# Kernel optimization log

Hardware: AMD Instinct MI355X
Metric: run time of the kernel (lower is better)

The kernel has to match this reference:

```python
import jax, jax.numpy as jnp
from jax import lax
import numpy as np

EPS = 1e-5

def _conv_bn(x, w, g, b, m, v):
    # 3x3 VALID conv (no bias) + inference BatchNorm, no relu
    y = lax.conv_general_dilated(x, w, window_strides=(1, 1), padding='VALID',
                                 dimension_numbers=('NCHW', 'OIHW', 'NCHW'))
    inv = g * lax.rsqrt(v + EPS)                      # [C]
    return y * inv[None, :, None, None] + (b - m * inv)[None, :, None, None]

def _xcorr_depthwise(z, x):
    # z: [B,C,hz,wz] kernel, x: [B,C,hx,wx] search -> [B,C,hx-hz+1,wx-wz+1]
    C = z.shape[1]
    def one(zi, xi):
        return lax.conv_general_dilated(xi[None], zi[:, None], (1, 1), 'VALID',
                                        dimension_numbers=('NCHW', 'OIHW', 'NCHW'),
                                        feature_group_count=C)[0]
    return jax.vmap(one)(z, x)

def setup_inputs() -> dict:
    key = jax.random.key(0)
    B, Cin, H = 32, 256, 256
    ks = jax.random.split(key, 30)
    d = {
        'z': jax.random.normal(ks[0], (B, Cin, 8, 8), jnp.float32),
        'x': jax.random.normal(ks[1], (B, Cin, 32, 32), jnp.float32),
    }
    i = 2
    for p in ['cls_z', 'cls_x', 'reg_z', 'reg_x']:
        d[p + '_w'] = 0.01 * jax.random.normal(ks[i], (H, Cin, 3, 3), jnp.float32); i += 1
        d[p + '_g'] = jnp.ones((H,), jnp.float32)
        d[p + '_b'] = jnp.zeros((H,), jnp.float32)
        d[p + '_m'] = 0.1 * jax.random.normal(ks[i], (H,), jnp.float32); i += 1
        d[p + '_v'] = jax.random.uniform(ks[i], (H,), jnp.float32, 0.5, 1.5); i += 1
    return d

def reference(z, x,
              cls_z_w, cls_z_g, cls_z_b, cls_z_m, cls_z_v,
              cls_x_w, cls_x_g, cls_x_b, cls_x_m, cls_x_v,
              reg_z_w, reg_z_g, reg_z_b, reg_z_m, reg_z_v,
              reg_x_w, reg_x_g, reg_x_b, reg_x_m, reg_x_v):
    cls_z = _conv_bn(z, cls_z_w, cls_z_g, cls_z_b, cls_z_m, cls_z_v)
    cls_x = _conv_bn(x, cls_x_w, cls_x_g, cls_x_b, cls_x_m, cls_x_v)
    cls_out = _xcorr_depthwise(cls_z, cls_x)
    reg_z = _conv_bn(z, reg_z_w, reg_z_g, reg_z_b, reg_z_m, reg_z_v)
    reg_x = _conv_bn(x, reg_x_w, reg_x_g, reg_x_b, reg_x_m, reg_x_v)
    reg_out = _xcorr_depthwise(reg_z, reg_x)
    return (cls_out, reg_out)
```

## Files before the change

### kernel.cpp

```cpp
#include <hip/hip_runtime.h>

#define EPS 1e-5f

typedef __attribute__((ext_vector_type(8))) short bf16x8;
typedef __attribute__((ext_vector_type(4))) float f32x4;
typedef __attribute__((ext_vector_type(4))) unsigned short u16x4;
typedef unsigned short ushort_t;

__device__ __forceinline__ ushort_t f2bf(float f) {
  unsigned u = __float_as_uint(f);
  unsigned r = (u + 0x7fffu + ((u >> 16) & 1u)) >> 16;
  return (ushort_t)r;
}
__device__ __forceinline__ float bf2f(ushort_t h) {
  return __uint_as_float((unsigned)h << 16);
}

#define GLDS16(g, l) __builtin_amdgcn_global_load_lds( \
    (const __attribute__((address_space(1))) void*)(g), \
    (__attribute__((address_space(3))) void*)(l), 16, 0, 0)

__global__ __launch_bounds__(256) void pack_kernel(
    const float* __restrict__ x, const float* __restrict__ z,
    const float* __restrict__ wxa, const float* __restrict__ wxb,
    const float* __restrict__ wza, const float* __restrict__ wzb,
    ushort_t* __restrict__ xh, ushort_t* __restrict__ zh,
    ushort_t* __restrict__ Bxo, ushort_t* __restrict__ Bzo)
{
  __shared__ ushort_t t[256 * 66];
  int id = blockIdx.x;
  int tid = threadIdx.x;
  if (id < 1024) {
    int b = id >> 5, h = id & 31;
    const float* src = x + (size_t)b * 256 * 1024 + h * 32;
#pragma unroll
    for (int it = 0; it < 32; ++it) {
      int f = it * 256 + tid;
      int c = f >> 5, w = f & 31;
      t[c * 34 + w] = f2bf(src[c * 1024 + w]);
    }
    __syncthreads();
    ushort_t* dst = xh + (size_t)(b * 32 + h) * 32 * 256;
#pragma unroll
    for (int it = 0; it < 32; ++it) {
      int f = it * 256 + tid;
      int w = f >> 8, c = f & 255;
      dst[w * 256 + c] = t[c * 34 + w];
    }
  } else if (id < 1056) {
    int b = id - 1024;
    const float* src = z + (size_t)b * 256 * 64;
#pragma unroll
    for (int it = 0; it < 64; ++it) {
      int f = it * 256 + tid;
      int c = f >> 6, hw = f & 63;
      t[c * 66 + hw] = f2bf(src[c * 64 + hw]);
    }
    __syncthreads();
    ushort_t* dst = zh + (size_t)b * 64 * 256;
#pragma unroll
    for (int it = 0; it < 64; ++it) {
      int f = it * 256 + tid;
      int hw = f >> 8, c = f & 255;
      dst[hw * 256 + c] = t[c * 66 + hw];
    }
  } else {
    int wid = id - 1056;
    int isZ = wid >> 9;
    int n   = wid & 511;
    const float* s0 = isZ ? wza : wxa;
    const float* s1 = isZ ? wzb : wxb;
    const float* src = (n < 256 ? s0 : s1) + (size_t)(n & 255) * 2304 + tid * 9;
    ushort_t* dst = (isZ ? Bzo : Bxo) + (size_t)n * 2304 + tid;
#pragma unroll
    for (int tap = 0; tap < 9; ++tap)
      dst[tap * 256] = f2bf(src[tap]);
  }
}

template<int OW, int OWH, int IW, int IMG, typename OutT>
__device__ __forceinline__ void conv_body(
    int mtile, int ntile,
    const ushort_t* __restrict__ Aimg, const ushort_t* __restrict__ Bw,
    const float* __restrict__ g0, const float* __restrict__ b0,
    const float* __restrict__ m0, const float* __restrict__ v0,
    const float* __restrict__ g1, const float* __restrict__ b1,
    const float* __restrict__ m1, const float* __restrict__ v1,
    OutT* __restrict__ out0, OutT* __restrict__ out1,
    ushort_t* As, ushort_t* Bs)
{
  const int tid  = threadIdx.x;
  const int lane = tid & 63;
  const int wave = tid >> 6;
  const int wr   = wave >> 1, wc = wave & 1;

  const int chunk = (tid & 7) ^ ((tid >> 3) & 7);
  int abase[4], bbase[4];
#pragma unroll
  for (int i = 0; i < 4; ++i) {
    int row = i * 32 + (tid >> 3);
    int m_g = mtile * 128 + row;
    int b   = m_g / OWH;
    int s   = m_g - b * OWH;
    int oh  = s / OW;
    int ow  = s - oh * OW;
    abase[i] = (b * IMG + oh * IW + ow) * 256 + chunk * 8;
    int n_g = ntile * 128 + row;
    bbase[i] = n_g * 2304 + chunk * 8;
  }

  f32x4 acc[4][4];
#pragma unroll
  for (int i = 0; i < 4; ++i)
#pragma unroll
    for (int j = 0; j < 4; ++j)
      acc[i][j] = (f32x4){0.f, 0.f, 0.f, 0.f};

  const int lrow = lane & 15;
  const int lk   = lane >> 4;
  const int rA   = wr * 64;
  const int rB   = wc * 64;
  const int sw   = lrow & 7;

  for (int ks = 0; ks < 36; ++ks) {
    const int k0  = ks * 64;
    const int tap = k0 >> 8;
    const int ci0 = k0 & 255;
    const int kh  = tap / 3;
    const int kw  = tap - kh * 3;
    const int aoff = (kh * IW + kw) * 256 + ci0;
#pragma unroll
    for (int i = 0; i < 4; ++i) {
      GLDS16(Aimg + abase[i] + aoff, &As[(i * 256 + tid) * 8]);
      GLDS16(Bw + bbase[i] + k0,     &Bs[(i * 256 + tid) * 8]);
    }
    __syncthreads();
#pragma unroll
    for (int kc = 0; kc < 2; ++kc) {
      bf16x8 af[4], bfr[4];
#pragma unroll
      for (int mi = 0; mi < 4; ++mi)
        af[mi] = *(const bf16x8*)&As[(rA + mi * 16 + lrow) * 64 + (((kc << 2) | lk) ^ sw) * 8];
#pragma unroll
      for (int ni = 0; ni < 4; ++ni)
        bfr[ni] = *(const bf16x8*)&Bs[(rB + ni * 16 + lrow) * 64 + (((kc << 2) | lk) ^ sw) * 8];
#pragma unroll
      for (int mi = 0; mi < 4; ++mi)
#pragma unroll
        for (int ni = 0; ni < 4; ++ni)
          acc[mi][ni] = __builtin_amdgcn_mfma_f32_16x16x32_bf16(
              af[mi], bfr[ni], acc[mi][ni], 0, 0, 0);
    }
    __syncthreads();
  }

#pragma unroll
  for (int ni = 0; ni < 4; ++ni) {
    int n_g  = ntile * 128 + rB + ni * 16 + lrow;
    int path = n_g >> 8;
    int co   = n_g & 255;
    const float* G  = path ? g1 : g0;
    const float* Bb = path ? b1 : b0;
    const float* Mm = path ? m1 : m0;
    const float* Vv = path ? v1 : v0;
    float iv = G[co] * rsqrtf(Vv[co] + EPS);
    float be = Bb[co] - Mm[co] * iv;
    OutT* outp = path ? out1 : out0;
#pragma unroll
    for (int mi = 0; mi < 4; ++mi) {
      int m_g = mtile * 128 + rA + mi * 16 + lk * 4;
      int b   = m_g / OWH;
      int s   = m_g - b * OWH;
      if constexpr (sizeof(OutT) == 2) {
        u16x4 pk;
#pragma unroll
        for (int r = 0; r < 4; ++r) pk[r] = f2bf(acc[mi][ni][r] * iv + be);
        *reinterpret_cast<u16x4*>(&outp[(size_t)(b * 256 + co) * OWH + s]) = pk;
      } else {
        f32x4 pk;
#pragma unroll
        for (int r = 0; r < 4; ++r) pk[r] = acc[mi][ni][r] * iv + be;
        *reinterpret_cast<f32x4*>(&outp[(size_t)(b * 256 + co) * OWH + s]) = pk;
      }
    }
  }
}

__global__ __launch_bounds__(256) void conv_fused_kernel(
    const ushort_t* __restrict__ xh, const ushort_t* __restrict__ zh,
    const ushort_t* __restrict__ Bx, const ushort_t* __restrict__ Bz,
    const float* Gcx, const float* Bcx, const float* Mcx, const float* Vcx,
    const float* Grx, const float* Brx, const float* Mrx, const float* Vrx,
    const float* Gcz, const float* Bcz, const float* Mcz, const float* Vcz,
    const float* Grz, const float* Brz, const float* Mrz, const float* Vrz,
    ushort_t* __restrict__ cls_xf, ushort_t* __restrict__ reg_xf,
    float* __restrict__ cls_zf, float* __restrict__ reg_zf)
{
  __shared__ ushort_t As[128 * 64];
  __shared__ ushort_t Bs[128 * 64];
  int id = blockIdx.x;
  if (id < 900) {
    conv_body<30, 900, 32, 1024, ushort_t>(id >> 2, id & 3, xh, Bx,
        Gcx, Bcx, Mcx, Vcx, Grx, Brx, Mrx, Vrx, cls_xf, reg_xf, As, Bs);
  } else {
    int j = id - 900;
    conv_body<6, 36, 8, 64, float>(j >> 2, j & 3, zh, Bz,
        Gcz, Bcz, Mcz, Vcz, Grz, Brz, Mrz, Vrz, cls_zf, reg_zf, As, Bs);
  }
}

__global__ __launch_bounds__(256) void xcorr_kernel(
    const float* __restrict__ cls_zf, const float* __restrict__ reg_zf,
    const ushort_t* __restrict__ cls_xf, const ushort_t* __restrict__ reg_xf,
    float* __restrict__ out)
{
  int id   = blockIdx.x;
  int path = id >> 13;
  int bc   = id & 8191;
  int tid  = threadIdx.x;
  __shared__ float sz[36];
  __shared__ float sx[900];
  const float*    zp = (path ? reg_zf : cls_zf) + (size_t)bc * 36;
  const ushort_t* xp = (path ? reg_xf : cls_xf) + (size_t)bc * 900;
  const unsigned* xp32 = reinterpret_cast<const unsigned*>(xp);
  for (int i = tid; i < 450; i += 256) {
    unsigned u = xp32[i];
    sx[2 * i]     = bf2f((ushort_t)(u & 0xffff));
    sx[2 * i + 1] = bf2f((ushort_t)(u >> 16));
  }
  if (tid < 36) sz[tid] = zp[tid];
  __syncthreads();
  float* op = out + (size_t)path * 5120000 + (size_t)bc * 625;
  for (int pos = tid; pos < 625; pos += 256) {
    int p = pos / 25, q = pos % 25;
    float acc = 0.f;
#pragma unroll
    for (int u = 0; u < 6; ++u)
#pragma unroll
      for (int v = 0; v < 6; ++v)
        acc += sz[u * 6 + v] * sx[(p + u) * 30 + (q + v)];
    op[pos] = acc;
  }
}

extern "C" void kernel_launch(void* const* d_in, const int* in_sizes, int n_in,
                              void* d_out, int out_size, void* d_ws, size_t ws_size,
                              hipStream_t stream) {
  const float* z = (const float*)d_in[0];
  const float* x = (const float*)d_in[1];
  const float *W[4], *G[4], *Bb[4], *M[4], *V[4];
  for (int p = 0; p < 4; ++p) {
    W[p]  = (const float*)d_in[2 + p * 5 + 0];
    G[p]  = (const float*)d_in[2 + p * 5 + 1];
    Bb[p] = (const float*)d_in[2 + p * 5 + 2];
    M[p]  = (const float*)d_in[2 + p * 5 + 3];
    V[p]  = (const float*)d_in[2 + p * 5 + 4];
  }

  char* ws = (char*)d_ws;
  ushort_t* xhwc   = (ushort_t*)ws; ws += (size_t)32*32*32*256 * 2;
  ushort_t* zhwc   = (ushort_t*)ws; ws += (size_t)32*8*8*256 * 2;
  ushort_t* Bx     = (ushort_t*)ws; ws += (size_t)512*2304 * 2;
  ushort_t* Bz     = (ushort_t*)ws; ws += (size_t)512*2304 * 2;
  ushort_t* cls_xf = (ushort_t*)ws; ws += (size_t)32*256*900 * 2;
  ushort_t* reg_xf = (ushort_t*)ws; ws += (size_t)32*256*900 * 2;
  float* cls_zf    = (float*)ws;    ws += (size_t)32*256*36 * 4;
  float* reg_zf    = (float*)ws;

  float* outF = (float*)d_out;

  pack_kernel<<<2080, 256, 0, stream>>>(x, z, W[1], W[3], W[0], W[2],
                                        xhwc, zhwc, Bx, Bz);
  conv_fused_kernel<<<936, 256, 0, stream>>>(
      xhwc, zhwc, Bx, Bz,
      G[1], Bb[1], M[1], V[1], G[3], Bb[3], M[3], V[3],
      G[0], Bb[0], M[0], V[0], G[2], Bb[2], M[2], V[2],
      cls_xf, reg_xf, cls_zf, reg_zf);
  xcorr_kernel<<<16384, 256, 0, stream>>>(cls_zf, reg_zf, cls_xf, reg_xf, outF);
}
```

Measured before the change: 277.6 us.

## Vectorize pack transposes, swizzle conv blocks across XCDs, register-cache xcorr kernel

```diff
diff --git a/kernel.cpp b/kernel.cpp
--- a/kernel.cpp
+++ b/kernel.cpp
@@ -27,54 +27,77 @@
     ushort_t* __restrict__ xh, ushort_t* __restrict__ zh,
     ushort_t* __restrict__ Bxo, ushort_t* __restrict__ Bzo)
 {
-  __shared__ ushort_t t[256 * 66];
+  __shared__ ushort_t t[64 * 260];
   int id = blockIdx.x;
   int tid = threadIdx.x;
   if (id < 1024) {
     int b = id >> 5, h = id & 31;
-    const float* src = x + (size_t)b * 256 * 1024 + h * 32;
-#pragma unroll
-    for (int it = 0; it < 32; ++it) {
+    const float* src = x + (size_t)b * 262144 + h * 32;
+#pragma unroll
+    for (int it = 0; it < 8; ++it) {
       int f = it * 256 + tid;
-      int c = f >> 5, w = f & 31;
-      t[c * 34 + w] = f2bf(src[c * 1024 + w]);
-    }
-    __syncthreads();
-    ushort_t* dst = xh + (size_t)(b * 32 + h) * 32 * 256;
-#pragma unroll
-    for (int it = 0; it < 32; ++it) {
-      int f = it * 256 + tid;
-      int w = f >> 8, c = f & 255;
-      dst[w * 256 + c] = t[c * 34 + w];
+      int c = f >> 3, wq = f & 7;
+      float4 v = *reinterpret_cast<const float4*>(src + c * 1024 + wq * 4);
+      t[(4 * wq + 0) * 260 + c] = f2bf(v.x);
+      t[(4 * wq + 1) * 260 + c] = f2bf(v.y);
+      t[(4 * wq + 2) * 260 + c] = f2bf(v.z);
+      t[(4 * wq + 3) * 260 + c] = f2bf(v.w);
+    }
+    __syncthreads();
+    ushort_t* dst = xh + (size_t)(b * 32 + h) * 8192;
+#pragma unroll
+    for (int it = 0; it < 8; ++it) {
+      int Q = it * 256 + tid;
+      int w = Q >> 6, c0 = (Q & 63) * 4;
+      u16x4 pk = *reinterpret_cast<const u16x4*>(&t[w * 260 + c0]);
+      *reinterpret_cast<u16x4*>(&dst[w * 256 + c0]) = pk;
     }
   } else if (id < 1056) {
     int b = id - 1024;
-    const float* src = z + (size_t)b * 256 * 64;
-#pragma unroll
-    for (int it = 0; it < 64; ++it) {
+    const float* src = z + (size_t)b * 16384;
+#pragma unroll
+    for (int it = 0; it < 16; ++it) {
       int f = it * 256 + tid;
-      int c = f >> 6, hw = f & 63;
-      t[c * 66 + hw] = f2bf(src[c * 64 + hw]);
-    }
-    __syncthreads();
-    ushort_t* dst = zh + (size_t)b * 64 * 256;
-#pragma unroll
-    for (int it = 0; it < 64; ++it) {
-      int f = it * 256 + tid;
-      int hw = f >> 8, c = f & 255;
-      dst[hw * 256 + c] = t[c * 66 + hw];
+      int c = f >> 4, hq = f & 15;
+      float4 v = *reinterpret_cast<const float4*>(src + c * 64 + hq * 4);
+      t[(4 * hq + 0) * 260 + c] = f2bf(v.x);
+      t[(4 * hq + 1) * 260 + c] = f2bf(v.y);
+      t[(4 * hq + 2) * 260 + c] = f2bf(v.z);
+      t[(4 * hq + 3) * 260 + c] = f2bf(v.w);
+    }
+    __syncthreads();
+    ushort_t* dst = zh + (size_t)b * 16384;
+#pragma unroll
+    for (int it = 0; it < 16; ++it) {
+      int Q = it * 256 + tid;
+      int hw = Q >> 6, c0 = (Q & 63) * 4;
+      u16x4 pk = *reinterpret_cast<const u16x4*>(&t[hw * 260 + c0]);
+      *reinterpret_cast<u16x4*>(&dst[hw * 256 + c0]) = pk;
     }
   } else {
+    float* tf = reinterpret_cast<float*>(t);
     int wid = id - 1056;
     int isZ = wid >> 9;
     int n   = wid & 511;
     const float* s0 = isZ ? wza : wxa;
     const float* s1 = isZ ? wzb : wxb;
-    const float* src = (n < 256 ? s0 : s1) + (size_t)(n & 255) * 2304 + tid * 9;
-    ushort_t* dst = (isZ ? Bzo : Bxo) + (size_t)n * 2304 + tid;
-#pragma unroll
-    for (int tap = 0; tap < 9; ++tap)
-      dst[tap * 256] = f2bf(src[tap]);
+    const float* src = (n < 256 ? s0 : s1) + (size_t)(n & 255) * 2304;
+#pragma unroll
+    for (int it = 0; it < 3; ++it) {
+      int f = it * 256 + tid;
+      if (f < 576) {
+        float4 v = *reinterpret_cast<const float4*>(src + f * 4);
+        *reinterpret_cast<float4*>(&tf[f * 4]) = v;
+      }
+    }
+    __syncthreads();
+    ushort_t* dst = (isZ ? Bzo : Bxo) + (size_t)n * 2304;
+#pragma unroll
+    for (int it = 0; it < 9; ++it) {
+      int k = it * 256 + tid;
+      int tap = k >> 8, ci = k & 255;
+      dst[k] = f2bf(tf[ci * 9 + tap]);
+    }
   }
 }
 
@@ -198,12 +221,14 @@
 {
   __shared__ ushort_t As[128 * 64];
   __shared__ ushort_t Bs[128 * 64];
-  int id = blockIdx.x;
-  if (id < 900) {
+  int bid = blockIdx.x;
+  if (bid < 900) {
+    int xcd = bid & 7, within = bid >> 3;
+    int id = (xcd < 4 ? xcd * 113 : 452 + (xcd - 4) * 112) + within;
     conv_body<30, 900, 32, 1024, ushort_t>(id >> 2, id & 3, xh, Bx,
         Gcx, Bcx, Mcx, Vcx, Grx, Brx, Mrx, Vrx, cls_xf, reg_xf, As, Bs);
   } else {
-    int j = id - 900;
+    int j = bid - 900;
     conv_body<6, 36, 8, 64, float>(j >> 2, j & 3, zh, Bz,
         Gcz, Bcz, Mcz, Vcz, Grz, Brz, Mrz, Vrz, cls_zf, reg_zf, As, Bs);
   }
@@ -218,18 +243,22 @@
   int path = id >> 13;
   int bc   = id & 8191;
   int tid  = threadIdx.x;
-  __shared__ float sz[36];
+  __shared__ float szs[36];
   __shared__ float sx[900];
   const float*    zp = (path ? reg_zf : cls_zf) + (size_t)bc * 36;
   const ushort_t* xp = (path ? reg_xf : cls_xf) + (size_t)bc * 900;
-  const unsigned* xp32 = reinterpret_cast<const unsigned*>(xp);
-  for (int i = tid; i < 450; i += 256) {
-    unsigned u = xp32[i];
-    sx[2 * i]     = bf2f((ushort_t)(u & 0xffff));
-    sx[2 * i + 1] = bf2f((ushort_t)(u >> 16));
-  }
-  if (tid < 36) sz[tid] = zp[tid];
+  if (tid < 225) {
+    u16x4 v = *reinterpret_cast<const u16x4*>(xp + tid * 4);
+    sx[tid * 4 + 0] = bf2f(v[0]);
+    sx[tid * 4 + 1] = bf2f(v[1]);
+    sx[tid * 4 + 2] = bf2f(v[2]);
+    sx[tid * 4 + 3] = bf2f(v[3]);
+  }
+  if (tid < 36) szs[tid] = zp[tid];
   __syncthreads();
+  float zreg[36];
+#pragma unroll
+  for (int i = 0; i < 36; ++i) zreg[i] = szs[i];
   float* op = out + (size_t)path * 5120000 + (size_t)bc * 625;
   for (int pos = tid; pos < 625; pos += 256) {
     int p = pos / 25, q = pos % 25;
@@ -238,7 +267,7 @@
     for (int u = 0; u < 6; ++u)
 #pragma unroll
       for (int v = 0; v < 6; ++v)
-        acc += sz[u * 6 + v] * sx[(p + u) * 30 + (q + v)];
+        acc += zreg[u * 6 + v] * sx[(p + u) * 30 + (q + v)];
     op[pos] = acc;
   }
 }
```

Measured after the change: 268.0 us. -3.5%, faster.
